# Kernel optimization log

Measured on AMD Instinct MI355X. Metric: run time of the kernel, lower is better.

## Reference

```python
import jax, jax.numpy as jnp
import numpy as np

N_NODES = 100000
N_EDGES = 1600000
F_IN = 128
HID = 128
N_CLS = 40


def setup_inputs() -> dict:
    key = jax.random.key(0)
    ks = jax.random.split(key, 8)
    x = jax.random.normal(ks[0], (N_NODES, F_IN), dtype=jnp.float32)
    edge_index = jax.random.randint(ks[1], (2, N_EDGES), 0, N_NODES, dtype=jnp.int32)
    s1 = 1.0 / np.sqrt(F_IN)
    s2 = 1.0 / np.sqrt(HID)
    W1 = jax.random.normal(ks[2], (F_IN, HID), dtype=jnp.float32) * s1
    b1 = jnp.zeros((HID,), dtype=jnp.float32)
    W2 = jax.random.normal(ks[3], (HID, HID), dtype=jnp.float32) * s2
    b2 = jnp.zeros((HID,), dtype=jnp.float32)
    Wout = jax.random.normal(ks[4], (HID, N_CLS), dtype=jnp.float32) * s2
    bout = jnp.zeros((N_CLS,), dtype=jnp.float32)
    return {"x": x, "edge_index": edge_index, "W1": W1, "b1": b1,
            "W2": W2, "b2": b2, "Wout": Wout, "bout": bout}


def gcn_conv(x, W, b, src, dst, n_nodes):
    """PyG-style GCNConv: h = D^-1/2 (A + I) D^-1/2 (x W) + b."""
    h = x @ W  # [N, H]
    # degree including self-loop
    deg = jnp.zeros((n_nodes,), dtype=h.dtype).at[dst].add(1.0) + 1.0
    dinv = jax.lax.rsqrt(deg)  # [N]
    coeff = dinv[src] * dinv[dst]  # [E]
    msgs = h[src] * coeff[:, None]  # [E, H] gathered messages
    agg = jnp.zeros_like(h).at[dst].add(msgs)
    # self-loop contribution: norm = dinv[i]^2
    agg = agg + h * (dinv * dinv)[:, None]
    return agg + b


def reference(x, edge_index, W1, b1, W2, b2, Wout, bout):
    src, dst = edge_index[0], edge_index[1]
    n = x.shape[0]
    h = jax.nn.relu(gcn_conv(x, W1, b1, src, dst, n))
    # dropout is identity in eval mode
    h = jax.nn.relu(gcn_conv(h, W2, b2, src, dst, n))
    return h @ Wout + bout
```

## Files before the change

kernel.cpp:

```cpp
#include <hip/hip_runtime.h>
#include <hip/hip_bf16.h>
#include <hip/hip_fp16.h>

#define NNODES 100000
#define NEDGES 1600000
#define FD 128
#define NCLS 40
#define DEGCAP 128
#define NBIN 256
#define BINW2 391
#define CAPB2 8192
#define SUBC 1024
#define SBLK 4096

typedef __attribute__((ext_vector_type(8))) _Float16 half8;
typedef __attribute__((ext_vector_type(4))) float floatx4;

__device__ __forceinline__ float4 h4_to_f4(int2 p) {
    __half2 a = __builtin_bit_cast(__half2, p.x);
    __half2 b = __builtin_bit_cast(__half2, p.y);
    float2 fa = __half22float2(a), fb = __half22float2(b);
    return make_float4(fa.x, fa.y, fb.x, fb.y);
}

__device__ __forceinline__ void pack_one(const float* __restrict__ W, int ncols,
                                         int nt_count, short* __restrict__ out,
                                         int id) {
    int lane = id & 63;
    int nt = (id >> 6) % nt_count;
    int ko = id / (64 * nt_count);
    int col = nt * 16 + (lane & 15);
    int kbase = ko * 32 + (lane >> 4) * 8;
    short* dst = out + (size_t)id * 16;
    #pragma unroll
    for (int j = 0; j < 8; ++j) {
        float v = (col < ncols) ? W[(size_t)(kbase + j) * ncols + col] : 0.f;
        _Float16 h = (_Float16)v;
        _Float16 l = (_Float16)(v - (float)h);
        dst[j] = __builtin_bit_cast(short, h);
        dst[8 + j] = __builtin_bit_cast(short, l);
    }
}

__global__ __launch_bounds__(256) void prep(const float* __restrict__ W1,
                                            const float* __restrict__ W2,
                                            const float* __restrict__ Wout,
                                            short* __restrict__ w1pk,
                                            short* __restrict__ w2pk,
                                            short* __restrict__ wopk,
                                            int* __restrict__ cursor) {
    int id = blockIdx.x * blockDim.x + threadIdx.x;
    if (id < 2048) pack_one(W1, FD, 8, w1pk, id);
    else if (id < 4096) pack_one(W2, FD, 8, w2pk, id - 2048);
    else if (id < 4864) pack_one(Wout, NCLS, 3, wopk, id - 4096);
    else if (id < 6912) {
        int c = id - 4864;
        cursor[c] = (c >> 3) * CAPB2 + (c & 7) * SUBC;
    }
}

__global__ __launch_bounds__(256) void scatter_k(const int* __restrict__ src,
                                                 const int* __restrict__ dst,
                                                 int* __restrict__ cursor,
                                                 int* __restrict__ ebin) {
    __shared__ int lh[4][NBIN];
    __shared__ int obase[4][NBIN];
    int t = threadIdx.x, wv = t >> 6;
    int g = blockIdx.x & 7;
    int base = blockIdx.x * SBLK;
    for (int i = t; i < 4 * NBIN; i += 256) ((int*)lh)[i] = 0;
    __syncthreads();
    int pay[16];
    unsigned short binv[16], rankv[16];
    #pragma unroll
    for (int i = 0; i < 16; ++i) {
        int idx = base + t + i * 256;
        int b = 0, r = 0, p = -1;
        if (idx < NEDGES) {
            int d = dst[idx];
            b = d / BINW2;
            p = src[idx] | ((d - b * BINW2) << 17);
            r = atomicAdd(&lh[wv][b], 1);
        }
        pay[i] = p; binv[i] = (unsigned short)b; rankv[i] = (unsigned short)r;
    }
    __syncthreads();
    if (t < NBIN) {
        int c0 = lh[0][t], c1 = lh[1][t], c2 = lh[2][t], c3 = lh[3][t];
        int tot = c0 + c1 + c2 + c3;
        int gb = tot ? atomicAdd(&cursor[t * 8 + g], tot) : 0;
        obase[0][t] = gb;
        obase[1][t] = gb + c0;
        obase[2][t] = gb + c0 + c1;
        obase[3][t] = gb + c0 + c1 + c2;
    }
    __syncthreads();
    #pragma unroll
    for (int i = 0; i < 16; ++i) {
        if (pay[i] != -1) {
            int b = binv[i];
            int pos = obase[wv][b] + rankv[i];
            if (pos < b * CAPB2 + (g + 1) * SUBC)
                ebin[pos] = pay[i];
        }
    }
}

__global__ __launch_bounds__(256) void build_bin(const int* __restrict__ ebin,
                                                 const int* __restrict__ cursor,
                                                 int* __restrict__ adj,
                                                 int* __restrict__ rowptr,
                                                 int* __restrict__ degA,
                                                 float* __restrict__ dinv) {
    __shared__ int stage[CAPB2];
    __shared__ int hist[BINW2 + 1];
    __shared__ int rp[BINW2 + 1];
    int bin = blockIdx.x, t = threadIdx.x;
    int off = 0;
    #pragma unroll
    for (int x = 0; x < 8; ++x) {
        int sb = bin * CAPB2 + x * SUBC;
        int nex = cursor[bin * 8 + x] - sb;
        if (nex > SUBC) nex = SUBC;
        for (int i = t; i < nex; i += 256) stage[off + i] = ebin[sb + i];
        off += nex;
    }
    int ne = off;
    for (int i = t; i < BINW2 + 1; i += 256) hist[i] = 0;
    __syncthreads();
    for (int i = t; i < ne; i += 256) atomicAdd(&hist[stage[i] >> 17], 1);
    __syncthreads();
    if (t < 64) {
        int c[7]; int s = 0;
        #pragma unroll
        for (int k = 0; k < 7; ++k) {
            int idx = t * 7 + k;
            c[k] = (idx < BINW2) ? hist[idx] : 0;
            s += c[k];
        }
        int inc = s;
        #pragma unroll
        for (int o = 1; o < 64; o <<= 1) {
            int v = __shfl_up(inc, o);
            if (t >= o) inc += v;
        }
        int excl = inc - s;
        #pragma unroll
        for (int k = 0; k < 7; ++k) {
            int idx = t * 7 + k;
            if (idx < BINW2) { rp[idx] = excl; excl += c[k]; }
        }
    }
    __syncthreads();
    int nbase = bin * BINW2;
    for (int l = t; l < BINW2; l += 256) {
        int node = nbase + l;
        if (node < NNODES) {
            rowptr[node] = bin * CAPB2 + rp[l];
            int dg = hist[l];
            degA[node] = dg;
            dinv[node] = rsqrtf((float)dg + 1.0f);
        }
    }
    __syncthreads();
    for (int i = t; i < BINW2 + 1; i += 256) hist[i] = 0;
    __syncthreads();
    for (int i = t; i < ne; i += 256) {
        int p = stage[i];
        int loc = p >> 17;
        int r = atomicAdd(&hist[loc], 1);
        adj[bin * CAPB2 + rp[loc] + r] = p & 0x1FFFF;
    }
}

__global__ __launch_bounds__(512) void gemm_mfma128_h(const float* __restrict__ X,
                                                      const short* __restrict__ Bpk,
                                                      const float* __restrict__ dinv,
                                                      __half* __restrict__ Y) {
    __shared__ short bs[2048 * 16];
    {
        const int4* s = (const int4*)Bpk;
        int4* d = (int4*)bs;
        for (int i = threadIdx.x; i < 4096; i += 512) d[i] = s[i];
    }
    __syncthreads();
    int w = threadIdx.x >> 6, lane = threadIdx.x & 63;
    int quad = lane >> 4, m = lane & 15;
    int row0 = blockIdx.x * 128 + w * 16;
    int arow = row0 + m;
    bool aok = arow < NNODES;
    floatx4 acc[8];
    #pragma unroll
    for (int nt = 0; nt < 8; ++nt) acc[nt] = (floatx4){0.f, 0.f, 0.f, 0.f};
    #pragma unroll
    for (int ko = 0; ko < 4; ++ko) {
        int kbase = ko * 32 + quad * 8;
        float4 a0 = aok ? *(const float4*)(X + (size_t)arow * FD + kbase)
                        : make_float4(0.f, 0.f, 0.f, 0.f);
        float4 a1 = aok ? *(const float4*)(X + (size_t)arow * FD + kbase + 4)
                        : make_float4(0.f, 0.f, 0.f, 0.f);
        float f[8] = {a0.x, a0.y, a0.z, a0.w, a1.x, a1.y, a1.z, a1.w};
        half8 ahi, alo;
        #pragma unroll
        for (int j = 0; j < 8; ++j) {
            ahi[j] = (_Float16)f[j];
            alo[j] = (_Float16)(f[j] - (float)ahi[j]);
        }
        const short* bp = bs + (size_t)(ko * 8) * 64 * 16 + (size_t)lane * 16;
        #pragma unroll
        for (int nt = 0; nt < 8; ++nt) {
            half8 bhi = *(const half8*)bp;
            half8 blo = *(const half8*)(bp + 8);
            bp += 64 * 16;
            acc[nt] = __builtin_amdgcn_mfma_f32_16x16x32_f16(ahi, bhi, acc[nt], 0, 0, 0);
            acc[nt] = __builtin_amdgcn_mfma_f32_16x16x32_f16(ahi, blo, acc[nt], 0, 0, 0);
            acc[nt] = __builtin_amdgcn_mfma_f32_16x16x32_f16(alo, bhi, acc[nt], 0, 0, 0);
        }
    }
    #pragma unroll
    for (int r = 0; r < 4; ++r) {
        int rr = row0 + quad * 4 + r;
        if (rr < NNODES) {
            float sc = dinv[rr];
            __half* y = Y + (size_t)rr * FD + m;
            #pragma unroll
            for (int nt = 0; nt < 8; ++nt) y[nt * 16] = __float2half(acc[nt][r] * sc);
        }
    }
}

__global__ __launch_bounds__(512) void gemm_mfma128_hh(const __half* __restrict__ X,
                                                       const short* __restrict__ Bpk,
                                                       const float* __restrict__ dinv,
                                                       __half* __restrict__ Y) {
    __shared__ short bs[2048 * 16];
    {
        const int4* s = (const int4*)Bpk;
        int4* d = (int4*)bs;
        for (int i = threadIdx.x; i < 4096; i += 512) d[i] = s[i];
    }
    __syncthreads();
    int w = threadIdx.x >> 6, lane = threadIdx.x & 63;
    int quad = lane >> 4, m = lane & 15;
    int row0 = blockIdx.x * 128 + w * 16;
    int arow = row0 + m;
    bool aok = arow < NNODES;
    floatx4 acc[8];
    #pragma unroll
    for (int nt = 0; nt < 8; ++nt) acc[nt] = (floatx4){0.f, 0.f, 0.f, 0.f};
    #pragma unroll
    for (int ko = 0; ko < 4; ++ko) {
        int kbase = ko * 32 + quad * 8;
        int4 ar = aok ? *(const int4*)(X + (size_t)arow * FD + kbase)
                      : make_int4(0, 0, 0, 0);
        half8 a = __builtin_bit_cast(half8, ar);
        const short* bp = bs + (size_t)(ko * 8) * 64 * 16 + (size_t)lane * 16;
        #pragma unroll
        for (int nt = 0; nt < 8; ++nt) {
            half8 bhi = *(const half8*)bp;
            half8 blo = *(const half8*)(bp + 8);
            bp += 64 * 16;
            acc[nt] = __builtin_amdgcn_mfma_f32_16x16x32_f16(a, bhi, acc[nt], 0, 0, 0);
            acc[nt] = __builtin_amdgcn_mfma_f32_16x16x32_f16(a, blo, acc[nt], 0, 0, 0);
        }
    }
    #pragma unroll
    for (int r = 0; r < 4; ++r) {
        int rr = row0 + quad * 4 + r;
        if (rr < NNODES) {
            float sc = dinv[rr];
            __half* y = Y + (size_t)rr * FD + m;
            #pragma unroll
            for (int nt = 0; nt < 8; ++nt) y[nt * 16] = __float2half(acc[nt][r] * sc);
        }
    }
}

__global__ __launch_bounds__(512) void gemm_out_mfma_h(const __half* __restrict__ X,
                                                       const short* __restrict__ Bpk,
                                                       const float* __restrict__ bout,
                                                       float* __restrict__ Y) {
    __shared__ short bs[768 * 16];
    {
        const int4* s = (const int4*)Bpk;
        int4* d = (int4*)bs;
        for (int i = threadIdx.x; i < 1536; i += 512) d[i] = s[i];
    }
    __syncthreads();
    int w = threadIdx.x >> 6, lane = threadIdx.x & 63;
    int quad = lane >> 4, m = lane & 15;
    int row0 = blockIdx.x * 128 + w * 16;
    int arow = row0 + m;
    bool aok = arow < NNODES;
    floatx4 acc[3];
    #pragma unroll
    for (int nt = 0; nt < 3; ++nt) acc[nt] = (floatx4){0.f, 0.f, 0.f, 0.f};
    #pragma unroll
    for (int ko = 0; ko < 4; ++ko) {
        int kbase = ko * 32 + quad * 8;
        int4 ar = aok ? *(const int4*)(X + (size_t)arow * FD + kbase)
                      : make_int4(0, 0, 0, 0);
        half8 a = __builtin_bit_cast(half8, ar);
        const short* bp = bs + (size_t)(ko * 3) * 64 * 16 + (size_t)lane * 16;
        #pragma unroll
        for (int nt = 0; nt < 3; ++nt) {
            half8 bhi = *(const half8*)bp;
            half8 blo = *(const half8*)(bp + 8);
            bp += 64 * 16;
            acc[nt] = __builtin_amdgcn_mfma_f32_16x16x32_f16(a, bhi, acc[nt], 0, 0, 0);
            acc[nt] = __builtin_amdgcn_mfma_f32_16x16x32_f16(a, blo, acc[nt], 0, 0, 0);
        }
    }
    #pragma unroll
    for (int r = 0; r < 4; ++r) {
        int rr = row0 + quad * 4 + r;
        if (rr < NNODES) {
            #pragma unroll
            for (int nt = 0; nt < 3; ++nt) {
                int col = nt * 16 + m;
                if (col < NCLS)
                    Y[(size_t)rr * NCLS + col] = acc[nt][r] + bout[col];
            }
        }
    }
}

__global__ __launch_bounds__(128) void aggregate_h2(const int2* __restrict__ XW2,
                                                    const int* __restrict__ rowptr,
                                                    const int* __restrict__ degA,
                                                    const int* __restrict__ adj,
                                                    const float* __restrict__ dinv,
                                                    const float* __restrict__ bias,
                                                    int2* __restrict__ Yh) {
    __shared__ int ssrc[4][DEGCAP];
    int sub  = threadIdx.x >> 5;
    int lane = threadIdx.x & 31;
    int node = blockIdx.x * 4 + sub;
    float di = dinv[node];
    int deg = degA[node];
    if (deg > DEGCAP) deg = DEGCAP;
    int base = rowptr[node];
    for (int j = lane; j < deg; j += 32)
        ssrc[sub][j] = adj[base + j];
    __syncthreads();
    float4 b = *(const float4*)(bias + 4 * lane);
    float4 acc = h4_to_f4(XW2[(size_t)node * 32 + lane]);
    int j = 0;
    for (; j + 7 < deg; j += 8) {
        int2 p[8];
        #pragma unroll
        for (int q = 0; q < 8; ++q)
            p[q] = XW2[(size_t)ssrc[sub][j + q] * 32 + lane];
        #pragma unroll
        for (int q = 0; q < 8; ++q) {
            float4 vq = h4_to_f4(p[q]);
            acc.x += vq.x; acc.y += vq.y; acc.z += vq.z; acc.w += vq.w;
        }
    }
    for (; j < deg; ++j) {
        float4 v0 = h4_to_f4(XW2[(size_t)ssrc[sub][j] * 32 + lane]);
        acc.x += v0.x; acc.y += v0.y; acc.z += v0.z; acc.w += v0.w;
    }
    __half2 h01 = __floats2half2_rn(fmaxf(fmaf(acc.x, di, b.x), 0.f),
                                    fmaxf(fmaf(acc.y, di, b.y), 0.f));
    __half2 h23 = __floats2half2_rn(fmaxf(fmaf(acc.z, di, b.z), 0.f),
                                    fmaxf(fmaf(acc.w, di, b.w), 0.f));
    Yh[(size_t)node * 32 + lane] = make_int2(__builtin_bit_cast(int, h01),
                                             __builtin_bit_cast(int, h23));
}

extern "C" void kernel_launch(void* const* d_in, const int* in_sizes, int n_in,
                              void* d_out, int out_size, void* d_ws, size_t ws_size,
                              hipStream_t stream) {
    const float* x    = (const float*)d_in[0];
    const int*   ei   = (const int*)d_in[1];
    const float* W1   = (const float*)d_in[2];
    const float* b1   = (const float*)d_in[3];
    const float* W2   = (const float*)d_in[4];
    const float* b2   = (const float*)d_in[5];
    const float* Wout = (const float*)d_in[6];
    const float* bout = (const float*)d_in[7];
    float* out = (float*)d_out;

    const int* srcv = ei;
    const int* dstv = ei + NEDGES;

    float* bufA   = (float*)d_ws;
    float* bufB   = bufA + (size_t)NNODES * FD;
    int*   adj    = (int*)(bufB + (size_t)NNODES * FD);
    int*   rowptr = adj + (size_t)NBIN * CAPB2;
    int*   degA   = rowptr + NNODES;
    float* dinv   = (float*)(degA + NNODES);
    short* w1pk   = (short*)(dinv + NNODES);
    short* w2pk   = w1pk + 2048 * 16;
    short* wopk   = w2pk + 2048 * 16;
    int*   cursor = (int*)(wopk + 768 * 16);
    int*   ebin   = (int*)bufA;
    __half* xwh   = (__half*)bufA;
    __half* acth  = (__half*)bufB;

    prep<<<27, 256, 0, stream>>>(W1, W2, Wout, w1pk, w2pk, wopk, cursor);

    scatter_k<<<(NEDGES + SBLK - 1) / SBLK, 256, 0, stream>>>(srcv, dstv, cursor, ebin);
    build_bin<<<NBIN, 256, 0, stream>>>(ebin, cursor, adj, rowptr, degA, dinv);

    const int gblocks = (NNODES + 127) / 128;
    gemm_mfma128_h<<<gblocks, 512, 0, stream>>>(x, w1pk, dinv, xwh);
    aggregate_h2<<<NNODES / 4, 128, 0, stream>>>((const int2*)xwh, rowptr, degA,
                                                 adj, dinv, b1, (int2*)acth);
    gemm_mfma128_hh<<<gblocks, 512, 0, stream>>>(acth, w2pk, dinv, xwh);
    aggregate_h2<<<NNODES / 4, 128, 0, stream>>>((const int2*)xwh, rowptr, degA,
                                                 adj, dinv, b2, (int2*)acth);
    gemm_out_mfma_h<<<gblocks, 512, 0, stream>>>(acth, wopk, bout, out);
}
```

Measured before the change: 309.5 us.

## Fuse weight packing into scatter and CSR build into first GEMM launch

Merges the weight-packing prep kernel into the edge scatter kernel as extra blocks, and merges the per-bin CSR build with the first feature GEMM into one launch. Degrees are now counted with global atomics during the scatter so the GEMM can compute its normalisation without waiting for the bin build. Cursor and degree arrays are cleared with memsets, and the edge staging buffer moves so it no longer aliases the GEMM output. This removes launches and serialisation between stages, at the cost of 1.6M extra global atomics and a larger shared-memory footprint per block.

```diff
diff --git a/kernel.cpp b/kernel.cpp
--- a/kernel.cpp
+++ b/kernel.cpp
@@ -12,6 +12,8 @@
 #define CAPB2 8192
 #define SUBC 1024
 #define SBLK 4096
+#define SCBLK ((NEDGES + SBLK - 1) / SBLK)
+#define PRBLK 19
 
 typedef __attribute__((ext_vector_type(8))) _Float16 half8;
 typedef __attribute__((ext_vector_type(4))) float floatx4;
@@ -42,27 +44,24 @@
     }
 }
 
-__global__ __launch_bounds__(256) void prep(const float* __restrict__ W1,
-                                            const float* __restrict__ W2,
-                                            const float* __restrict__ Wout,
-                                            short* __restrict__ w1pk,
-                                            short* __restrict__ w2pk,
-                                            short* __restrict__ wopk,
-                                            int* __restrict__ cursor) {
-    int id = blockIdx.x * blockDim.x + threadIdx.x;
-    if (id < 2048) pack_one(W1, FD, 8, w1pk, id);
-    else if (id < 4096) pack_one(W2, FD, 8, w2pk, id - 2048);
-    else if (id < 4864) pack_one(Wout, NCLS, 3, wopk, id - 4096);
-    else if (id < 6912) {
-        int c = id - 4864;
-        cursor[c] = (c >> 3) * CAPB2 + (c & 7) * SUBC;
-    }
-}
-
-__global__ __launch_bounds__(256) void scatter_k(const int* __restrict__ src,
-                                                 const int* __restrict__ dst,
-                                                 int* __restrict__ cursor,
-                                                 int* __restrict__ ebin) {
+__global__ __launch_bounds__(256) void scatter_prep(const int* __restrict__ src,
+                                                    const int* __restrict__ dst,
+                                                    int* __restrict__ cursor,
+                                                    int* __restrict__ ebin,
+                                                    int* __restrict__ degA,
+                                                    const float* __restrict__ W1,
+                                                    const float* __restrict__ W2,
+                                                    const float* __restrict__ Wout,
+                                                    short* __restrict__ w1pk,
+                                                    short* __restrict__ w2pk,
+                                                    short* __restrict__ wopk) {
+    if (blockIdx.x >= SCBLK) {
+        int id = (blockIdx.x - SCBLK) * 256 + threadIdx.x;
+        if (id < 2048) pack_one(W1, FD, 8, w1pk, id);
+        else if (id < 4096) pack_one(W2, FD, 8, w2pk, id - 2048);
+        else if (id < 4864) pack_one(Wout, NCLS, 3, wopk, id - 4096);
+        return;
+    }
     __shared__ int lh[4][NBIN];
     __shared__ int obase[4][NBIN];
     int t = threadIdx.x, wv = t >> 6;
@@ -81,6 +80,7 @@
             b = d / BINW2;
             p = src[idx] | ((d - b * BINW2) << 17);
             r = atomicAdd(&lh[wv][b], 1);
+            atomicAdd(&degA[d], 1);
         }
         pay[i] = p; binv[i] = (unsigned short)b; rankv[i] = (unsigned short)r;
     }
@@ -99,94 +99,94 @@
     for (int i = 0; i < 16; ++i) {
         if (pay[i] != -1) {
             int b = binv[i];
-            int pos = obase[wv][b] + rankv[i];
-            if (pos < b * CAPB2 + (g + 1) * SUBC)
-                ebin[pos] = pay[i];
-        }
-    }
-}
-
-__global__ __launch_bounds__(256) void build_bin(const int* __restrict__ ebin,
-                                                 const int* __restrict__ cursor,
-                                                 int* __restrict__ adj,
-                                                 int* __restrict__ rowptr,
-                                                 int* __restrict__ degA,
-                                                 float* __restrict__ dinv) {
-    __shared__ int stage[CAPB2];
-    __shared__ int hist[BINW2 + 1];
-    __shared__ int rp[BINW2 + 1];
-    int bin = blockIdx.x, t = threadIdx.x;
-    int off = 0;
-    #pragma unroll
-    for (int x = 0; x < 8; ++x) {
-        int sb = bin * CAPB2 + x * SUBC;
-        int nex = cursor[bin * 8 + x] - sb;
-        if (nex > SUBC) nex = SUBC;
-        for (int i = t; i < nex; i += 256) stage[off + i] = ebin[sb + i];
-        off += nex;
-    }
-    int ne = off;
-    for (int i = t; i < BINW2 + 1; i += 256) hist[i] = 0;
-    __syncthreads();
-    for (int i = t; i < ne; i += 256) atomicAdd(&hist[stage[i] >> 17], 1);
-    __syncthreads();
-    if (t < 64) {
-        int c[7]; int s = 0;
-        #pragma unroll
-        for (int k = 0; k < 7; ++k) {
-            int idx = t * 7 + k;
-            c[k] = (idx < BINW2) ? hist[idx] : 0;
-            s += c[k];
-        }
-        int inc = s;
-        #pragma unroll
-        for (int o = 1; o < 64; o <<= 1) {
-            int v = __shfl_up(inc, o);
-            if (t >= o) inc += v;
-        }
-        int excl = inc - s;
-        #pragma unroll
-        for (int k = 0; k < 7; ++k) {
-            int idx = t * 7 + k;
-            if (idx < BINW2) { rp[idx] = excl; excl += c[k]; }
-        }
-    }
-    __syncthreads();
-    int nbase = bin * BINW2;
-    for (int l = t; l < BINW2; l += 256) {
-        int node = nbase + l;
-        if (node < NNODES) {
-            rowptr[node] = bin * CAPB2 + rp[l];
-            int dg = hist[l];
-            degA[node] = dg;
-            dinv[node] = rsqrtf((float)dg + 1.0f);
-        }
-    }
-    __syncthreads();
-    for (int i = t; i < BINW2 + 1; i += 256) hist[i] = 0;
-    __syncthreads();
-    for (int i = t; i < ne; i += 256) {
-        int p = stage[i];
-        int loc = p >> 17;
-        int r = atomicAdd(&hist[loc], 1);
-        adj[bin * CAPB2 + rp[loc] + r] = p & 0x1FFFF;
-    }
-}
-
-__global__ __launch_bounds__(512) void gemm_mfma128_h(const float* __restrict__ X,
-                                                      const short* __restrict__ Bpk,
-                                                      const float* __restrict__ dinv,
-                                                      __half* __restrict__ Y) {
-    __shared__ short bs[2048 * 16];
+            int rel = obase[wv][b] + rankv[i];
+            if (rel < SUBC)
+                ebin[b * CAPB2 + g * SUBC + rel] = pay[i];
+        }
+    }
+}
+
+__global__ __launch_bounds__(512) void build_gemm1(const int* __restrict__ ebin,
+                                                   const int* __restrict__ cursor,
+                                                   int* __restrict__ adj,
+                                                   int* __restrict__ rowptr,
+                                                   const int* __restrict__ degA,
+                                                   float* __restrict__ dinv,
+                                                   const float* __restrict__ X,
+                                                   const short* __restrict__ Bpk,
+                                                   __half* __restrict__ Y) {
+    __shared__ __align__(16) char smem[65536];
+    int t = threadIdx.x;
+    if (blockIdx.x < NBIN) {
+        int* stage = (int*)smem;
+        int* hist  = (int*)(smem + CAPB2 * 4);
+        int* rp    = (int*)(smem + CAPB2 * 4 + (BINW2 + 1) * 4);
+        int bin = blockIdx.x;
+        int off = 0;
+        #pragma unroll
+        for (int x = 0; x < 8; ++x) {
+            int nex = cursor[bin * 8 + x];
+            if (nex > SUBC) nex = SUBC;
+            const int* sb = ebin + bin * CAPB2 + x * SUBC;
+            for (int i = t; i < nex; i += 512) stage[off + i] = sb[i];
+            off += nex;
+        }
+        int ne = off;
+        for (int i = t; i < BINW2 + 1; i += 512) hist[i] = 0;
+        __syncthreads();
+        for (int i = t; i < ne; i += 512) atomicAdd(&hist[stage[i] >> 17], 1);
+        __syncthreads();
+        if (t < 64) {
+            int c[7]; int s = 0;
+            #pragma unroll
+            for (int k = 0; k < 7; ++k) {
+                int idx = t * 7 + k;
+                c[k] = (idx < BINW2) ? hist[idx] : 0;
+                s += c[k];
+            }
+            int inc = s;
+            #pragma unroll
+            for (int o = 1; o < 64; o <<= 1) {
+                int v = __shfl_up(inc, o);
+                if (t >= o) inc += v;
+            }
+            int excl = inc - s;
+            #pragma unroll
+            for (int k = 0; k < 7; ++k) {
+                int idx = t * 7 + k;
+                if (idx < BINW2) { rp[idx] = excl; excl += c[k]; }
+            }
+        }
+        __syncthreads();
+        int nbase = bin * BINW2;
+        for (int l = t; l < BINW2; l += 512) {
+            int node = nbase + l;
+            if (node < NNODES) {
+                rowptr[node] = bin * CAPB2 + rp[l];
+                dinv[node] = rsqrtf((float)hist[l] + 1.0f);
+            }
+        }
+        __syncthreads();
+        for (int i = t; i < BINW2 + 1; i += 512) hist[i] = 0;
+        __syncthreads();
+        for (int i = t; i < ne; i += 512) {
+            int p = stage[i];
+            int loc = p >> 17;
+            int r = atomicAdd(&hist[loc], 1);
+            adj[bin * CAPB2 + rp[loc] + r] = p & 0x1FFFF;
+        }
+        return;
+    }
+    short* bs = (short*)smem;
     {
         const int4* s = (const int4*)Bpk;
-        int4* d = (int4*)bs;
-        for (int i = threadIdx.x; i < 4096; i += 512) d[i] = s[i];
-    }
-    __syncthreads();
-    int w = threadIdx.x >> 6, lane = threadIdx.x & 63;
+        int4* d = (int4*)smem;
+        for (int i = t; i < 4096; i += 512) d[i] = s[i];
+    }
+    __syncthreads();
+    int w = t >> 6, lane = t & 63;
     int quad = lane >> 4, m = lane & 15;
-    int row0 = blockIdx.x * 128 + w * 16;
+    int row0 = (blockIdx.x - NBIN) * 128 + w * 16;
     int arow = row0 + m;
     bool aok = arow < NNODES;
     floatx4 acc[8];
@@ -221,7 +221,7 @@
     for (int r = 0; r < 4; ++r) {
         int rr = row0 + quad * 4 + r;
         if (rr < NNODES) {
-            float sc = dinv[rr];
+            float sc = rsqrtf((float)degA[rr] + 1.0f);
             __half* y = Y + (size_t)rr * FD + m;
             #pragma unroll
             for (int nt = 0; nt < 8; ++nt) y[nt * 16] = __float2half(acc[nt][r] * sc);
@@ -395,17 +395,21 @@
     short* w2pk   = w1pk + 2048 * 16;
     short* wopk   = w2pk + 2048 * 16;
     int*   cursor = (int*)(wopk + 768 * 16);
-    int*   ebin   = (int*)bufA;
     __half* xwh   = (__half*)bufA;
+    int*   ebin   = (int*)(bufA + 6553600);
     __half* acth  = (__half*)bufB;
 
-    prep<<<27, 256, 0, stream>>>(W1, W2, Wout, w1pk, w2pk, wopk, cursor);
-
-    scatter_k<<<(NEDGES + SBLK - 1) / SBLK, 256, 0, stream>>>(srcv, dstv, cursor, ebin);
-    build_bin<<<NBIN, 256, 0, stream>>>(ebin, cursor, adj, rowptr, degA, dinv);
-
     const int gblocks = (NNODES + 127) / 128;
-    gemm_mfma128_h<<<gblocks, 512, 0, stream>>>(x, w1pk, dinv, xwh);
+
+    hipMemsetAsync(cursor, 0, NBIN * 8 * sizeof(int), stream);
+    hipMemsetAsync(degA, 0, NNODES * sizeof(int), stream);
+
+    scatter_prep<<<SCBLK + PRBLK, 256, 0, stream>>>(srcv, dstv, cursor, ebin, degA,
+                                                    W1, W2, Wout, w1pk, w2pk, wopk);
+
+    build_gemm1<<<NBIN + gblocks, 512, 0, stream>>>(ebin, cursor, adj, rowptr,
+                                                    degA, dinv, x, w1pk, xwh);
+
     aggregate_h2<<<NNODES / 4, 128, 0, stream>>>((const int2*)xwh, rowptr, degA,
                                                  adj, dinv, b1, (int2*)acth);
     gemm_mfma128_hh<<<gblocks, 512, 0, stream>>>(acth, w2pk, dinv, xwh);
```

Measured after the change: 355.8 us. +15.0%, slower.

## Replace binned CSR build with padded per-node adjacency via global atomics

Applied to the files above, without the earlier changes.

Drops the two-pass binned scatter plus per-bin CSR build and replaces it with one kernel. That kernel atomically increments a per-node counter and writes the source id into a fixed 64-slot row per destination node. Weight packing moves into extra blocks of the same launch. Degree and the inverse square root are now recomputed from the counter inside the GEMM and aggregation kernels. This removes kernels and intermediate passes, at the cost of 1.6M global atomics, a memset, and silently truncating any node with more than 64 in-edges.

```diff
diff --git a/kernel.cpp b/kernel.cpp
--- a/kernel.cpp
+++ b/kernel.cpp
@@ -6,12 +6,9 @@
 #define NEDGES 1600000
 #define FD 128
 #define NCLS 40
-#define DEGCAP 128
-#define NBIN 256
-#define BINW2 391
-#define CAPB2 8192
-#define SUBC 1024
-#define SBLK 4096
+#define DEGPAD 64
+#define SPBLK ((NEDGES + 255) / 256)
+#define PRBLK 19
 
 typedef __attribute__((ext_vector_type(8))) _Float16 half8;
 typedef __attribute__((ext_vector_type(4))) float floatx4;
@@ -42,140 +39,35 @@
     }
 }
 
-__global__ __launch_bounds__(256) void prep(const float* __restrict__ W1,
-                                            const float* __restrict__ W2,
-                                            const float* __restrict__ Wout,
-                                            short* __restrict__ w1pk,
-                                            short* __restrict__ w2pk,
-                                            short* __restrict__ wopk,
-                                            int* __restrict__ cursor) {
-    int id = blockIdx.x * blockDim.x + threadIdx.x;
-    if (id < 2048) pack_one(W1, FD, 8, w1pk, id);
-    else if (id < 4096) pack_one(W2, FD, 8, w2pk, id - 2048);
-    else if (id < 4864) pack_one(Wout, NCLS, 3, wopk, id - 4096);
-    else if (id < 6912) {
-        int c = id - 4864;
-        cursor[c] = (c >> 3) * CAPB2 + (c & 7) * SUBC;
-    }
-}
-
-__global__ __launch_bounds__(256) void scatter_k(const int* __restrict__ src,
-                                                 const int* __restrict__ dst,
-                                                 int* __restrict__ cursor,
-                                                 int* __restrict__ ebin) {
-    __shared__ int lh[4][NBIN];
-    __shared__ int obase[4][NBIN];
-    int t = threadIdx.x, wv = t >> 6;
-    int g = blockIdx.x & 7;
-    int base = blockIdx.x * SBLK;
-    for (int i = t; i < 4 * NBIN; i += 256) ((int*)lh)[i] = 0;
-    __syncthreads();
-    int pay[16];
-    unsigned short binv[16], rankv[16];
-    #pragma unroll
-    for (int i = 0; i < 16; ++i) {
-        int idx = base + t + i * 256;
-        int b = 0, r = 0, p = -1;
-        if (idx < NEDGES) {
-            int d = dst[idx];
-            b = d / BINW2;
-            p = src[idx] | ((d - b * BINW2) << 17);
-            r = atomicAdd(&lh[wv][b], 1);
-        }
-        pay[i] = p; binv[i] = (unsigned short)b; rankv[i] = (unsigned short)r;
-    }
-    __syncthreads();
-    if (t < NBIN) {
-        int c0 = lh[0][t], c1 = lh[1][t], c2 = lh[2][t], c3 = lh[3][t];
-        int tot = c0 + c1 + c2 + c3;
-        int gb = tot ? atomicAdd(&cursor[t * 8 + g], tot) : 0;
-        obase[0][t] = gb;
-        obase[1][t] = gb + c0;
-        obase[2][t] = gb + c0 + c1;
-        obase[3][t] = gb + c0 + c1 + c2;
-    }
-    __syncthreads();
-    #pragma unroll
-    for (int i = 0; i < 16; ++i) {
-        if (pay[i] != -1) {
-            int b = binv[i];
-            int pos = obase[wv][b] + rankv[i];
-            if (pos < b * CAPB2 + (g + 1) * SUBC)
-                ebin[pos] = pay[i];
-        }
-    }
-}
-
-__global__ __launch_bounds__(256) void build_bin(const int* __restrict__ ebin,
-                                                 const int* __restrict__ cursor,
-                                                 int* __restrict__ adj,
-                                                 int* __restrict__ rowptr,
-                                                 int* __restrict__ degA,
-                                                 float* __restrict__ dinv) {
-    __shared__ int stage[CAPB2];
-    __shared__ int hist[BINW2 + 1];
-    __shared__ int rp[BINW2 + 1];
-    int bin = blockIdx.x, t = threadIdx.x;
-    int off = 0;
-    #pragma unroll
-    for (int x = 0; x < 8; ++x) {
-        int sb = bin * CAPB2 + x * SUBC;
-        int nex = cursor[bin * 8 + x] - sb;
-        if (nex > SUBC) nex = SUBC;
-        for (int i = t; i < nex; i += 256) stage[off + i] = ebin[sb + i];
-        off += nex;
-    }
-    int ne = off;
-    for (int i = t; i < BINW2 + 1; i += 256) hist[i] = 0;
-    __syncthreads();
-    for (int i = t; i < ne; i += 256) atomicAdd(&hist[stage[i] >> 17], 1);
-    __syncthreads();
-    if (t < 64) {
-        int c[7]; int s = 0;
-        #pragma unroll
-        for (int k = 0; k < 7; ++k) {
-            int idx = t * 7 + k;
-            c[k] = (idx < BINW2) ? hist[idx] : 0;
-            s += c[k];
-        }
-        int inc = s;
-        #pragma unroll
-        for (int o = 1; o < 64; o <<= 1) {
-            int v = __shfl_up(inc, o);
-            if (t >= o) inc += v;
-        }
-        int excl = inc - s;
-        #pragma unroll
-        for (int k = 0; k < 7; ++k) {
-            int idx = t * 7 + k;
-            if (idx < BINW2) { rp[idx] = excl; excl += c[k]; }
-        }
-    }
-    __syncthreads();
-    int nbase = bin * BINW2;
-    for (int l = t; l < BINW2; l += 256) {
-        int node = nbase + l;
-        if (node < NNODES) {
-            rowptr[node] = bin * CAPB2 + rp[l];
-            int dg = hist[l];
-            degA[node] = dg;
-            dinv[node] = rsqrtf((float)dg + 1.0f);
-        }
-    }
-    __syncthreads();
-    for (int i = t; i < BINW2 + 1; i += 256) hist[i] = 0;
-    __syncthreads();
-    for (int i = t; i < ne; i += 256) {
-        int p = stage[i];
-        int loc = p >> 17;
-        int r = atomicAdd(&hist[loc], 1);
-        adj[bin * CAPB2 + rp[loc] + r] = p & 0x1FFFF;
+__global__ __launch_bounds__(256) void scatter_pad(const int* __restrict__ src,
+                                                   const int* __restrict__ dst,
+                                                   int* __restrict__ cnt,
+                                                   int* __restrict__ adj,
+                                                   const float* __restrict__ W1,
+                                                   const float* __restrict__ W2,
+                                                   const float* __restrict__ Wout,
+                                                   short* __restrict__ w1pk,
+                                                   short* __restrict__ w2pk,
+                                                   short* __restrict__ wopk) {
+    if (blockIdx.x >= SPBLK) {
+        int id = (blockIdx.x - SPBLK) * 256 + threadIdx.x;
+        if (id < 2048) pack_one(W1, FD, 8, w1pk, id);
+        else if (id < 4096) pack_one(W2, FD, 8, w2pk, id - 2048);
+        else if (id < 4864) pack_one(Wout, NCLS, 3, wopk, id - 4096);
+        return;
+    }
+    int idx = blockIdx.x * 256 + threadIdx.x;
+    if (idx < NEDGES) {
+        int d = dst[idx];
+        int r = atomicAdd(&cnt[d], 1);
+        if (r < DEGPAD)
+            adj[(size_t)d * DEGPAD + r] = src[idx];
     }
 }
 
 __global__ __launch_bounds__(512) void gemm_mfma128_h(const float* __restrict__ X,
                                                       const short* __restrict__ Bpk,
-                                                      const float* __restrict__ dinv,
+                                                      const int* __restrict__ cnt,
                                                       __half* __restrict__ Y) {
     __shared__ short bs[2048 * 16];
     {
@@ -221,7 +113,7 @@
     for (int r = 0; r < 4; ++r) {
         int rr = row0 + quad * 4 + r;
         if (rr < NNODES) {
-            float sc = dinv[rr];
+            float sc = rsqrtf((float)cnt[rr] + 1.0f);
             __half* y = Y + (size_t)rr * FD + m;
             #pragma unroll
             for (int nt = 0; nt < 8; ++nt) y[nt * 16] = __float2half(acc[nt][r] * sc);
@@ -231,7 +123,7 @@
 
 __global__ __launch_bounds__(512) void gemm_mfma128_hh(const __half* __restrict__ X,
                                                        const short* __restrict__ Bpk,
-                                                       const float* __restrict__ dinv,
+                                                       const int* __restrict__ cnt,
                                                        __half* __restrict__ Y) {
     __shared__ short bs[2048 * 16];
     {
@@ -268,7 +160,7 @@
     for (int r = 0; r < 4; ++r) {
         int rr = row0 + quad * 4 + r;
         if (rr < NNODES) {
-            float sc = dinv[rr];
+            float sc = rsqrtf((float)cnt[rr] + 1.0f);
             __half* y = Y + (size_t)rr * FD + m;
             #pragma unroll
             for (int nt = 0; nt < 8; ++nt) y[nt * 16] = __float2half(acc[nt][r] * sc);
@@ -326,22 +218,20 @@
 }
 
 __global__ __launch_bounds__(128) void aggregate_h2(const int2* __restrict__ XW2,
-                                                    const int* __restrict__ rowptr,
-                                                    const int* __restrict__ degA,
+                                                    const int* __restrict__ cnt,
                                                     const int* __restrict__ adj,
-                                                    const float* __restrict__ dinv,
                                                     const float* __restrict__ bias,
                                                     int2* __restrict__ Yh) {
-    __shared__ int ssrc[4][DEGCAP];
+    __shared__ int ssrc[4][DEGPAD];
     int sub  = threadIdx.x >> 5;
     int lane = threadIdx.x & 31;
     int node = blockIdx.x * 4 + sub;
-    float di = dinv[node];
-    int deg = degA[node];
-    if (deg > DEGCAP) deg = DEGCAP;
-    int base = rowptr[node];
+    int dg = cnt[node];
+    float di = rsqrtf((float)dg + 1.0f);
+    int deg = dg > DEGPAD ? DEGPAD : dg;
+    const int* base = adj + (size_t)node * DEGPAD;
     for (int j = lane; j < deg; j += 32)
-        ssrc[sub][j] = adj[base + j];
+        ssrc[sub][j] = base[j];
     __syncthreads();
     float4 b = *(const float4*)(bias + 4 * lane);
     float4 acc = h4_to_f4(XW2[(size_t)node * 32 + lane]);
@@ -387,29 +277,26 @@
 
     float* bufA   = (float*)d_ws;
     float* bufB   = bufA + (size_t)NNODES * FD;
-    int*   adj    = (int*)(bufB + (size_t)NNODES * FD);
-    int*   rowptr = adj + (size_t)NBIN * CAPB2;
-    int*   degA   = rowptr + NNODES;
-    float* dinv   = (float*)(degA + NNODES);
-    short* w1pk   = (short*)(dinv + NNODES);
+    int*   cnt    = (int*)(bufB + (size_t)NNODES * FD);
+    short* w1pk   = (short*)(cnt + NNODES);
     short* w2pk   = w1pk + 2048 * 16;
     short* wopk   = w2pk + 2048 * 16;
-    int*   cursor = (int*)(wopk + 768 * 16);
-    int*   ebin   = (int*)bufA;
     __half* xwh   = (__half*)bufA;
+    int*   adj    = (int*)(bufA + 6400000);
     __half* acth  = (__half*)bufB;
 
-    prep<<<27, 256, 0, stream>>>(W1, W2, Wout, w1pk, w2pk, wopk, cursor);
-
-    scatter_k<<<(NEDGES + SBLK - 1) / SBLK, 256, 0, stream>>>(srcv, dstv, cursor, ebin);
-    build_bin<<<NBIN, 256, 0, stream>>>(ebin, cursor, adj, rowptr, degA, dinv);
-
     const int gblocks = (NNODES + 127) / 128;
-    gemm_mfma128_h<<<gblocks, 512, 0, stream>>>(x, w1pk, dinv, xwh);
-    aggregate_h2<<<NNODES / 4, 128, 0, stream>>>((const int2*)xwh, rowptr, degA,
-                                                 adj, dinv, b1, (int2*)acth);
-    gemm_mfma128_hh<<<gblocks, 512, 0, stream>>>(acth, w2pk, dinv, xwh);
-    aggregate_h2<<<NNODES / 4, 128, 0, stream>>>((const int2*)xwh, rowptr, degA,
-                                                 adj, dinv, b2, (int2*)acth);
+
+    hipMemsetAsync(cnt, 0, NNODES * sizeof(int), stream);
+
+    scatter_pad<<<SPBLK + PRBLK, 256, 0, stream>>>(srcv, dstv, cnt, adj,
+                                                   W1, W2, Wout, w1pk, w2pk, wopk);
+
+    gemm_mfma128_h<<<gblocks, 512, 0, stream>>>(x, w1pk, cnt, xwh);
+    aggregate_h2<<<NNODES / 4, 128, 0, stream>>>((const int2*)xwh, cnt,
+                                                 adj, b1, (int2*)acth);
+    gemm_mfma128_hh<<<gblocks, 512, 0, stream>>>(acth, w2pk, cnt, xwh);
+    aggregate_h2<<<NNODES / 4, 128, 0, stream>>>((const int2*)xwh, cnt,
+                                                 adj, b2, (int2*)acth);
     gemm_out_mfma_h<<<gblocks, 512, 0, stream>>>(acth, wopk, bout, out);
 }
```

Measured after the change: 389.9 us. 26.0% more time.
